# Optimization experiments

Measured on AMD Instinct MI355X. Metric: run time of the kernel, lower is better.

The kernel has to match this reference:

```python
import jax, jax.numpy as jnp
import numpy as np

N_NODES = 50000
N_EDGES = 800000
N_GRAPHS = 128


def gcn_conv(x, row, col, W, b, num_nodes):
    # GCNConv: x' = D^-1/2 (A + I) D^-1/2 (x W) + b, with self-loops added.
    h = x @ W  # [N, out]
    # append self-loops
    sl = jnp.arange(num_nodes, dtype=row.dtype)
    r = jnp.concatenate([row, sl])
    c = jnp.concatenate([col, sl])
    deg = jax.ops.segment_sum(jnp.ones_like(r, dtype=h.dtype), r, num_segments=num_nodes)
    dinv = jnp.where(deg > 0, jax.lax.rsqrt(deg), 0.0)
    norm = dinv[r] * dinv[c]  # [E+N]
    msg = h[c] * norm[:, None]  # gather + scale
    out = jax.ops.segment_sum(msg, r, num_segments=num_nodes)
    return out + b


def setup_inputs() -> dict:
    key = jax.random.key(0)
    k = jax.random.split(key, 6)
    x = jax.random.normal(k[0], (N_NODES, 256), dtype=jnp.float32)
    edge_index = jax.random.randint(k[1], (2, N_EDGES), 0, N_NODES, dtype=jnp.int32)
    batch = jnp.sort(jax.random.randint(k[2], (N_NODES,), 0, N_GRAPHS, dtype=jnp.int32))
    W1 = jax.random.normal(k[3], (256, 128), dtype=jnp.float32) * (1.0 / np.sqrt(256))
    b1 = jnp.zeros((128,), dtype=jnp.float32)
    W2 = jax.random.normal(k[4], (128, 32), dtype=jnp.float32) * (1.0 / np.sqrt(128))
    b2 = jnp.zeros((32,), dtype=jnp.float32)
    return {"x": x, "edge_index": edge_index, "batch": batch,
            "W1": W1, "b1": b1, "W2": W2, "b2": b2}


def reference(x, edge_index, batch, W1, b1, W2, b2):
    row, col = edge_index[0], edge_index[1]
    h = gcn_conv(x, row, col, W1, b1, N_NODES)
    h = jax.nn.relu(h)
    # dropout is identity in eval mode (training=False)
    h = gcn_conv(h, row, col, W2, b2, N_NODES)
    # global_mean_pool over batch ids
    sums = jax.ops.segment_sum(h, batch, num_segments=N_GRAPHS)
    cnts = jax.ops.segment_sum(jnp.ones((N_NODES,), dtype=h.dtype), batch, num_segments=N_GRAPHS)
    pooled = sums / jnp.clip(cnts, 1.0)[:, None]  # [G, num_classes]
    return jax.nn.log_softmax(pooled, axis=1)
```

## Files before the change

kernel.cpp:

```cpp
#include <hip/hip_runtime.h>
#include <math.h>

#define N_NODES 50000
#define N_EDGES 800000
#define N_GRAPHS 128
#define DIM0 256
#define DIM1 128
#define DIM2 32

#define NBUCK 196
#define NEB 98

using f32x4 = __attribute__((ext_vector_type(4))) float;
using s16x8 = __attribute__((ext_vector_type(8))) short;

__device__ inline unsigned bf16pack(float a, float b) {
    unsigned ua = __float_as_uint(a), ub = __float_as_uint(b);
    ua = (ua + 0x7fffu + ((ua >> 16) & 1u)) >> 16;
    ub = (ub + 0x7fffu + ((ub >> 16) & 1u)) >> 16;
    return ua | (ub << 16);
}
__device__ inline float2 bf16x2(unsigned p) {
    return make_float2(__uint_as_float(p << 16), __uint_as_float(p & 0xffff0000u));
}

__global__ __launch_bounds__(256) void k_preph(const float* __restrict__ W1, uint* __restrict__ W1b,
                                               const int* __restrict__ batch, int* gstart,
                                               const int* __restrict__ row, int* __restrict__ hist) {
    __shared__ int h[NBUCK];
    int b = blockIdx.x, t = threadIdx.x;
    if (b < NEB) {
        if (t < NBUCK) h[t] = 0;
        __syncthreads();
#pragma unroll
        for (int i = 0; i < 8; ++i) {
            int idx = b * 2048 + i * 256 + t;
            if (idx < N_EDGES / 4) {
                int4 r4 = ((const int4*)row)[idx];
                atomicAdd(&h[r4.x >> 8], 1);
                atomicAdd(&h[r4.y >> 8], 1);
                atomicAdd(&h[r4.z >> 8], 1);
                atomicAdd(&h[r4.w >> 8], 1);
            }
        }
        __syncthreads();
        if (t < NBUCK) hist[b * NBUCK + t] = h[t];
    } else {
        int g = (b - NEB) * 256 + t;
        {
            int s = g >> 9, tt = (g >> 6) & 7, q = (g >> 4) & 3, n = g & 15;
            int k0 = s * 32 + q * 8;
            int col = tt * 16 + n;
            uint4 o;
            o.x = bf16pack(W1[(size_t)(k0 + 0) * DIM1 + col], W1[(size_t)(k0 + 1) * DIM1 + col]);
            o.y = bf16pack(W1[(size_t)(k0 + 2) * DIM1 + col], W1[(size_t)(k0 + 3) * DIM1 + col]);
            o.z = bf16pack(W1[(size_t)(k0 + 4) * DIM1 + col], W1[(size_t)(k0 + 5) * DIM1 + col]);
            o.w = bf16pack(W1[(size_t)(k0 + 6) * DIM1 + col], W1[(size_t)(k0 + 7) * DIM1 + col]);
            ((uint4*)W1b)[g] = o;
        }
        if (g <= N_GRAPHS) {
            int lo = 0, hi = N_NODES;
            while (lo < hi) { int mid = (lo + hi) >> 1; if (batch[mid] < g) lo = mid + 1; else hi = mid; }
            gstart[g] = lo;
        }
    }
}

__global__ __launch_bounds__(256) void k_place(const int* __restrict__ row, const int* __restrict__ col,
                                               const int* __restrict__ hist, uint* __restrict__ bb,
                                               int* __restrict__ bbase, int* __restrict__ btot) {
    __shared__ int cur[NBUCK];
    __shared__ int tot[NBUCK];
    __shared__ int sc[256];
    int blk = blockIdx.x, t = threadIdx.x;
    int pre = 0, to = 0;
    for (int b2 = 0; b2 < NEB; ++b2) {
        int v = (t < NBUCK) ? hist[b2 * NBUCK + t] : 0;
        to += v;
        if (b2 < blk) pre += v;
    }
    if (t < NBUCK) tot[t] = to;
    sc[t] = (t < NBUCK) ? to : 0;
    __syncthreads();
    for (int off = 1; off < 256; off <<= 1) {
        int x = (t >= off) ? sc[t - off] : 0;
        __syncthreads();
        sc[t] += x;
        __syncthreads();
    }
    if (t < NBUCK) {
        int base = sc[t] - tot[t];
        cur[t] = base + pre;
        if (blk == 0) { bbase[t] = base; btot[t] = tot[t]; }
    }
    __syncthreads();
#pragma unroll
    for (int i = 0; i < 8; ++i) {
        int idx = blk * 2048 + i * 256 + t;
        if (idx < N_EDGES / 4) {
            int4 r4 = ((const int4*)row)[idx];
            int4 c4 = ((const int4*)col)[idx];
            int rs[4] = {r4.x, r4.y, r4.z, r4.w};
            int cs[4] = {c4.x, c4.y, c4.z, c4.w};
#pragma unroll
            for (int j = 0; j < 4; ++j) {
                int pos = atomicAdd(&cur[rs[j] >> 8], 1);
                bb[pos] = ((uint)(rs[j] & 255) << 16) | (uint)cs[j];
            }
        }
    }
}

__global__ __launch_bounds__(256) void k_build(const int* __restrict__ bbase, const int* __restrict__ btot,
                                               const uint* __restrict__ bb,
                                               int* __restrict__ offs, int* __restrict__ cnt,
                                               ushort* __restrict__ csr) {
    __shared__ int c256[256];
    __shared__ int cur256[256];
    __shared__ int wsum[4];
    int b = blockIdx.x, t = threadIdx.x;
    int start = bbase[b];
    int n = btot[b];
    c256[t] = 0;
    __syncthreads();
    for (int i = t; i < n; i += 256) atomicAdd(&c256[bb[start + i] >> 16], 1);
    __syncthreads();
    int w = t >> 6, l = t & 63;
    int v = c256[t];
    int incl = v;
#pragma unroll
    for (int off = 1; off < 64; off <<= 1) {
        int x = __shfl_up(incl, off, 64);
        if (l >= off) incl += x;
    }
    if (l == 63) wsum[w] = incl;
    __syncthreads();
    int woff = 0;
    for (int i = 0; i < w; ++i) woff += wsum[i];
    int excl = incl - v + woff;
    cur256[t] = excl;
    int r = b * 256 + t;
    if (r < N_NODES) { offs[r] = start + excl; cnt[r] = v; }
    __syncthreads();
    for (int i = t; i < n; i += 256) {
        uint e = bb[start + i];
        int pos = atomicAdd(&cur256[e >> 16], 1);
        csr[start + pos] = (ushort)(e & 0xFFFFu);
    }
}

#define G1_BM 128
#define AS_LD 20
__global__ __launch_bounds__(256) void k_gemm1(const float* __restrict__ X, const uint* __restrict__ W1b,
                                               const int* __restrict__ cnt, unsigned* __restrict__ h1u) {
    __shared__ uint w1s[16384];
    __shared__ uint As[G1_BM * AS_LD];
    int t = threadIdx.x;
    int w = t >> 6, lane = t & 63, q = lane >> 4, m16 = lane & 15;
    int rowBase = blockIdx.x * G1_BM;

    {
        const uint4* src = (const uint4*)W1b;
        uint4* dst = (uint4*)w1s;
#pragma unroll
        for (int i = 0; i < 16; ++i) dst[i * 256 + t] = src[i * 256 + t];
    }

    f32x4 acc[2][8];
#pragma unroll
    for (int i = 0; i < 2; ++i)
#pragma unroll
        for (int j = 0; j < 8; ++j) acc[i][j] = (f32x4){0.f, 0.f, 0.f, 0.f};

    int ar = t >> 1, ah = t & 1;
    for (int s = 0; s < 8; ++s) {
        float4 f0 = {0,0,0,0}, f1 = {0,0,0,0}, f2 = {0,0,0,0}, f3 = {0,0,0,0};
        int grow = rowBase + ar;
        if (grow < N_NODES) {
            const float* src = X + (size_t)grow * DIM0 + s * 32 + ah * 16;
            f0 = *(const float4*)(src + 0);
            f1 = *(const float4*)(src + 4);
            f2 = *(const float4*)(src + 8);
            f3 = *(const float4*)(src + 12);
        }
        uint4 p0, p1;
        p0.x = bf16pack(f0.x, f0.y); p0.y = bf16pack(f0.z, f0.w);
        p0.z = bf16pack(f1.x, f1.y); p0.w = bf16pack(f1.z, f1.w);
        p1.x = bf16pack(f2.x, f2.y); p1.y = bf16pack(f2.z, f2.w);
        p1.z = bf16pack(f3.x, f3.y); p1.w = bf16pack(f3.z, f3.w);
        __syncthreads();
        *(uint4*)&As[ar * AS_LD + ah * 8 + 0] = p0;
        *(uint4*)&As[ar * AS_LD + ah * 8 + 4] = p1;
        __syncthreads();

        s16x8 af[2];
#pragma unroll
        for (int rt = 0; rt < 2; ++rt) {
            int arow = w * 32 + rt * 16 + m16;
            af[rt] = *(s16x8*)&As[arow * AS_LD + q * 4];
        }
#pragma unroll
        for (int tt = 0; tt < 8; ++tt) {
            s16x8 bf = *(s16x8*)&w1s[((s * 8 + tt) * 64 + lane) * 4];
            acc[0][tt] = __builtin_amdgcn_mfma_f32_16x16x32_bf16(af[0], bf, acc[0][tt], 0, 0, 0);
            acc[1][tt] = __builtin_amdgcn_mfma_f32_16x16x32_bf16(af[1], bf, acc[1][tt], 0, 0, 0);
        }
    }

#pragma unroll
    for (int rt = 0; rt < 2; ++rt) {
#pragma unroll
        for (int reg = 0; reg < 4; ++reg) {
            int row = rowBase + w * 32 + rt * 16 + q * 4 + reg;
            if (row < N_NODES) {
                float dv = rsqrtf((float)(cnt[row] + 1));
                unsigned* hr = h1u + (size_t)row * 64;
#pragma unroll
                for (int u = 0; u < 4; ++u)
                    hr[u * 16 + m16] = bf16pack(acc[rt][2 * u][reg] * dv, acc[rt][2 * u + 1][reg] * dv);
            }
        }
    }
}

__global__ __launch_bounds__(256) void k_agg1(const unsigned* __restrict__ h1u, const int* __restrict__ cnt,
                                              const int* __restrict__ offs, const ushort* __restrict__ csr,
                                              const float* __restrict__ b1, unsigned* __restrict__ a1u) {
    int node = blockIdx.x * 4 + (threadIdx.x >> 6);
    int lane = threadIdx.x & 63;
    float2 acc = bf16x2(h1u[(size_t)node * 64 + lane]);
    int n = cnt[node];
    const ushort* cp = csr + offs[node];
    {
        int ec = 0;
        if (lane < n) ec = cp[lane];
        int j = 0;
        for (; j + 8 <= n; j += 8) {
            int c0 = __shfl(ec, j),     c1 = __shfl(ec, j + 1), c2 = __shfl(ec, j + 2), c3 = __shfl(ec, j + 3);
            int c4 = __shfl(ec, j + 4), c5 = __shfl(ec, j + 5), c6 = __shfl(ec, j + 6), c7 = __shfl(ec, j + 7);
            unsigned p0 = h1u[(size_t)c0 * 64 + lane];
            unsigned p1 = h1u[(size_t)c1 * 64 + lane];
            unsigned p2 = h1u[(size_t)c2 * 64 + lane];
            unsigned p3 = h1u[(size_t)c3 * 64 + lane];
            unsigned p4 = h1u[(size_t)c4 * 64 + lane];
            unsigned p5 = h1u[(size_t)c5 * 64 + lane];
            unsigned p6 = h1u[(size_t)c6 * 64 + lane];
            unsigned p7 = h1u[(size_t)c7 * 64 + lane];
            float2 v0 = bf16x2(p0), v1 = bf16x2(p1), v2 = bf16x2(p2), v3 = bf16x2(p3);
            float2 v4 = bf16x2(p4), v5 = bf16x2(p5), v6 = bf16x2(p6), v7 = bf16x2(p7);
            acc.x += (v0.x + v1.x) + (v2.x + v3.x) + (v4.x + v5.x) + (v6.x + v7.x);
            acc.y += (v0.y + v1.y) + (v2.y + v3.y) + (v4.y + v5.y) + (v6.y + v7.y);
        }
        for (; j + 4 <= n; j += 4) {
            int c0 = __shfl(ec, j), c1 = __shfl(ec, j + 1), c2 = __shfl(ec, j + 2), c3 = __shfl(ec, j + 3);
            unsigned p0 = h1u[(size_t)c0 * 64 + lane];
            unsigned p1 = h1u[(size_t)c1 * 64 + lane];
            unsigned p2 = h1u[(size_t)c2 * 64 + lane];
            unsigned p3 = h1u[(size_t)c3 * 64 + lane];
            float2 v0 = bf16x2(p0), v1 = bf16x2(p1), v2 = bf16x2(p2), v3 = bf16x2(p3);
            acc.x += (v0.x + v1.x) + (v2.x + v3.x);
            acc.y += (v0.y + v1.y) + (v2.y + v3.y);
        }
        for (; j < n; ++j) {
            int c = __shfl(ec, j);
            float2 v = bf16x2(h1u[(size_t)c * 64 + lane]);
            acc.x += v.x; acc.y += v.y;
        }
    }
    float di = rsqrtf((float)(n + 1));
    int f0 = (lane >> 4) * 32 + (lane & 15);
    acc.x = fmaxf(acc.x * di + b1[f0], 0.f);
    acc.y = fmaxf(acc.y * di + b1[f0 + 16], 0.f);
    a1u[(size_t)node * 64 + lane] = bf16pack(acc.x, acc.y);
}

#define AS2_LD 132
__global__ __launch_bounds__(256) void k_gemm2(const unsigned* __restrict__ a1u, const float* __restrict__ W2,
                                               const int* __restrict__ cnt, unsigned* __restrict__ h2u) {
    __shared__ float As2[16 * AS2_LD];
    __shared__ float W2s[DIM1 * DIM2];
    int t = threadIdx.x;
    int rb = blockIdx.x * 16;
    {
        int r = t >> 4, cb = (t & 15) * 8;
        uint4 pv = *(const uint4*)(a1u + (size_t)(rb + r) * 64 + (t & 15) * 4);
        float2 u0 = bf16x2(pv.x), u1 = bf16x2(pv.y), u2 = bf16x2(pv.z), u3 = bf16x2(pv.w);
        float* dst = &As2[r * AS2_LD + cb];
        dst[0] = u0.x; dst[1] = u0.y; dst[2] = u1.x; dst[3] = u1.y;
        dst[4] = u2.x; dst[5] = u2.y; dst[6] = u3.x; dst[7] = u3.y;
    }
    for (int i = t; i < 1024; i += 256) {
        int k = i >> 3, c4 = (i & 7) * 4;
        int pos = 2 * ((k >> 5) * 16 + (k & 15)) + ((k >> 4) & 1);
        *(float4*)&W2s[pos * DIM2 + c4] = *(const float4*)(W2 + (size_t)k * DIM2 + c4);
    }
    __syncthreads();
    int r = t >> 4, c2 = (t & 15) * 2;
    float a0 = 0.f, a1v = 0.f;
#pragma unroll 8
    for (int k = 0; k < DIM1; ++k) {
        float a_ = As2[r * AS2_LD + k];
        a0  += a_ * W2s[k * DIM2 + c2];
        a1v += a_ * W2s[k * DIM2 + c2 + 1];
    }
    float dv = rsqrtf((float)(cnt[rb + r] + 1));
    h2u[(size_t)(rb + r) * 16 + (t & 15)] = bf16pack(a0 * dv, a1v * dv);
}

__global__ __launch_bounds__(256) void k_agg2(const unsigned* __restrict__ h2u, const int* __restrict__ cnt,
                                              const int* __restrict__ offs, const ushort* __restrict__ csr,
                                              const float* __restrict__ b2, float* __restrict__ a2) {
    int t = threadIdx.x;
    int node = blockIdx.x * 16 + (t >> 4);
    int l = t & 15;
    float2 acc = bf16x2(h2u[(size_t)node * 16 + l]);
    int n = cnt[node];
    const ushort* cp = csr + offs[node];
    for (int base = 0; base < n; base += 16) {
        int m = min(16, n - base);
        int ec = 0;
        if (l < m) ec = cp[base + l];
        int j = 0;
        for (; j + 4 <= m; j += 4) {
            int c0 = __shfl(ec, j, 16), c1 = __shfl(ec, j + 1, 16);
            int c2 = __shfl(ec, j + 2, 16), c3 = __shfl(ec, j + 3, 16);
            unsigned p0 = h2u[(size_t)c0 * 16 + l];
            unsigned p1 = h2u[(size_t)c1 * 16 + l];
            unsigned p2 = h2u[(size_t)c2 * 16 + l];
            unsigned p3 = h2u[(size_t)c3 * 16 + l];
            float2 v0 = bf16x2(p0), v1 = bf16x2(p1), v2 = bf16x2(p2), v3 = bf16x2(p3);
            acc.x += v0.x + v1.x + v2.x + v3.x;
            acc.y += v0.y + v1.y + v2.y + v3.y;
        }
        for (; j < m; ++j) {
            int c = __shfl(ec, j, 16);
            float2 v = bf16x2(h2u[(size_t)c * 16 + l]);
            acc.x += v.x; acc.y += v.y;
        }
    }
    float di = rsqrtf((float)(n + 1));
    acc.x = acc.x * di + b2[2 * l];
    acc.y = acc.y * di + b2[2 * l + 1];
    ((float2*)a2)[(size_t)node * 16 + l] = acc;
}

__global__ __launch_bounds__(256) void k_pool(const float* __restrict__ a2, const int* __restrict__ gstart,
                                              float* __restrict__ out) {
    __shared__ float sred[8][DIM2];
    int g = blockIdx.x;
    int t = threadIdx.x;
    int s = gstart[g], e = gstart[g + 1];
    int d = t & 31, r = t >> 5;
    float acc = 0.f;
    for (int i = s + r; i < e; i += 8) acc += a2[(size_t)i * DIM2 + d];
    sred[r][d] = acc;
    __syncthreads();
    if (t < DIM2) {
        float sum = 0.f;
#pragma unroll
        for (int j = 0; j < 8; ++j) sum += sred[j][t];
        float cntf = fmaxf((float)(e - s), 1.0f);
        float val = sum / cntf;
        float v = val;
#pragma unroll
        for (int m = 16; m >= 1; m >>= 1) v = fmaxf(v, __shfl_xor(v, m, 32));
        float ex = expf(val - v);
#pragma unroll
        for (int m = 16; m >= 1; m >>= 1) ex += __shfl_xor(ex, m, 32);
        out[g * DIM2 + t] = val - v - logf(ex);
    }
}

extern "C" void kernel_launch(void* const* d_in, const int* in_sizes, int n_in,
                              void* d_out, int out_size, void* d_ws, size_t ws_size,
                              hipStream_t stream) {
    const float* x     = (const float*)d_in[0];
    const int*   eidx  = (const int*)d_in[1];
    const int*   batch = (const int*)d_in[2];
    const float* W1    = (const float*)d_in[3];
    const float* b1    = (const float*)d_in[4];
    const float* W2    = (const float*)d_in[5];
    const float* b2    = (const float*)d_in[6];
    const int* row = eidx;
    const int* col = eidx + N_EDGES;
    float* out = (float*)d_out;

    char* p = (char*)d_ws;
    int*    cnt    = (int*)p;    p += (size_t)N_NODES * 4;
    int*    offs   = (int*)p;    p += (size_t)N_NODES * 4 + 16;
    int*    gstart = (int*)p;    p += 768;
    uint*   W1b    = (uint*)p;   p += 4096 * 16;
    int*    hist   = (int*)p;    p += (size_t)NEB * NBUCK * 4 + 32;
    int*    bbase  = (int*)p;    p += 1024;
    int*    btot   = (int*)p;    p += 1024;
    uint*   bb     = (uint*)p;   p += (size_t)N_EDGES * 4;
    ushort* csr    = (ushort*)p; p += (size_t)N_EDGES * 2;
    unsigned* h1u  = (unsigned*)p; p += (size_t)N_NODES * 64 * 4;
    unsigned* a1u  = (unsigned*)p; p += (size_t)N_NODES * 64 * 4;
    unsigned* h2u  = (unsigned*)p; p += (size_t)N_NODES * 16 * 4;
    float*  a2     = (float*)p;  p += (size_t)N_NODES * DIM2 * 4;

    k_preph<<<NEB + 16, 256, 0, stream>>>(W1, W1b, batch, gstart, row, hist);
    k_place<<<NEB, 256, 0, stream>>>(row, col, hist, bb, bbase, btot);
    k_build<<<NBUCK, 256, 0, stream>>>(bbase, btot, bb, offs, cnt, csr);

    k_gemm1<<<(N_NODES + G1_BM - 1) / G1_BM, 256, 0, stream>>>(x, W1b, cnt, h1u);
    k_agg1<<<N_NODES / 4, 256, 0, stream>>>(h1u, cnt, offs, csr, b1, a1u);
    k_gemm2<<<N_NODES / 16, 256, 0, stream>>>(a1u, W2, cnt, h2u);
    k_agg2<<<N_NODES / 16, 256, 0, stream>>>(h2u, cnt, offs, csr, b2, a2);
    k_pool<<<N_GRAPHS, 256, 0, stream>>>(a2, gstart, out);
}
```

Measured before the change: 225.8 us.

## Fuse layer-1 aggregation with layer-2 GEMM using bf16 MFMA

Merges k_agg1 and k_gemm2 into one kernel. Each block aggregates 16 nodes into an LDS tile, then one wave multiplies the tile by a pre-packed bf16 W2 using MFMA 16x16x32 instructions. This removes the a1u global round trip and one launch, and moves the second GEMM from scalar FP32 to bf16 MFMA. Output features come out permuted, so the agg2 bias indexing and the pool output write are remapped to match. Costs: 4x fewer, larger blocks for the aggregation and only one wave active during the GEMM phase.

Result: faster. 204.6 us (-9.4%).

```diff
diff --git a/kernel.cpp b/kernel.cpp
--- a/kernel.cpp
+++ b/kernel.cpp
@@ -24,7 +24,12 @@
     return make_float2(__uint_as_float(p << 16), __uint_as_float(p & 0xffff0000u));
 }
 
+__device__ inline int featOf(int p) {
+    return 32 * (p >> 5) + ((p >> 1) & 15) + 16 * (p & 1);
+}
+
 __global__ __launch_bounds__(256) void k_preph(const float* __restrict__ W1, uint* __restrict__ W1b,
+                                               const float* __restrict__ W2, uint* __restrict__ W2b,
                                                const int* __restrict__ batch, int* gstart,
                                                const int* __restrict__ row, int* __restrict__ hist) {
     __shared__ int h[NBUCK];
@@ -58,6 +63,17 @@
             o.w = bf16pack(W1[(size_t)(k0 + 6) * DIM1 + col], W1[(size_t)(k0 + 7) * DIM1 + col]);
             ((uint4*)W1b)[g] = o;
         }
+        if (g < 512) {
+            int s = g >> 7, tt = (g >> 6) & 1, l = g & 63;
+            int n = tt * 16 + (l & 15);
+            int kb = s * 32 + (l >> 4) * 8;
+            uint4 o;
+            o.x = bf16pack(W2[(size_t)featOf(kb + 0) * DIM2 + n], W2[(size_t)featOf(kb + 1) * DIM2 + n]);
+            o.y = bf16pack(W2[(size_t)featOf(kb + 2) * DIM2 + n], W2[(size_t)featOf(kb + 3) * DIM2 + n]);
+            o.z = bf16pack(W2[(size_t)featOf(kb + 4) * DIM2 + n], W2[(size_t)featOf(kb + 5) * DIM2 + n]);
+            o.w = bf16pack(W2[(size_t)featOf(kb + 6) * DIM2 + n], W2[(size_t)featOf(kb + 7) * DIM2 + n]);
+            ((uint4*)W2b)[g] = o;
+        }
         if (g <= N_GRAPHS) {
             int lo = 0, hi = N_NODES;
             while (lo < hi) { int mid = (lo + hi) >> 1; if (batch[mid] < g) lo = mid + 1; else hi = mid; }
@@ -223,15 +239,24 @@
     }
 }
 
-__global__ __launch_bounds__(256) void k_agg1(const unsigned* __restrict__ h1u, const int* __restrict__ cnt,
-                                              const int* __restrict__ offs, const ushort* __restrict__ csr,
-                                              const float* __restrict__ b1, unsigned* __restrict__ a1u) {
-    int node = blockIdx.x * 4 + (threadIdx.x >> 6);
-    int lane = threadIdx.x & 63;
-    float2 acc = bf16x2(h1u[(size_t)node * 64 + lane]);
-    int n = cnt[node];
-    const ushort* cp = csr + offs[node];
-    {
+#define A1_LD 68
+__global__ __launch_bounds__(256) void k_agg1g2(const unsigned* __restrict__ h1u, const int* __restrict__ cnt,
+                                                const int* __restrict__ offs, const ushort* __restrict__ csr,
+                                                const float* __restrict__ b1, const uint* __restrict__ W2b,
+                                                unsigned* __restrict__ h2u) {
+    __shared__ uint a1tile[16 * A1_LD];
+    __shared__ float sdi[16];
+    int t = threadIdx.x;
+    int wv = t >> 6, lane = t & 63;
+    int nb16 = blockIdx.x * 16;
+
+#pragma unroll
+    for (int i = 0; i < 4; ++i) {
+        int m = wv * 4 + i;
+        int node = nb16 + m;
+        float2 acc = bf16x2(h1u[(size_t)node * 64 + lane]);
+        int n = cnt[node];
+        const ushort* cp = csr + offs[node];
         int ec = 0;
         if (lane < n) ec = cp[lane];
         int j = 0;
@@ -266,45 +291,34 @@
             float2 v = bf16x2(h1u[(size_t)c * 64 + lane]);
             acc.x += v.x; acc.y += v.y;
         }
-    }
-    float di = rsqrtf((float)(n + 1));
-    int f0 = (lane >> 4) * 32 + (lane & 15);
-    acc.x = fmaxf(acc.x * di + b1[f0], 0.f);
-    acc.y = fmaxf(acc.y * di + b1[f0 + 16], 0.f);
-    a1u[(size_t)node * 64 + lane] = bf16pack(acc.x, acc.y);
-}
-
-#define AS2_LD 132
-__global__ __launch_bounds__(256) void k_gemm2(const unsigned* __restrict__ a1u, const float* __restrict__ W2,
-                                               const int* __restrict__ cnt, unsigned* __restrict__ h2u) {
-    __shared__ float As2[16 * AS2_LD];
-    __shared__ float W2s[DIM1 * DIM2];
-    int t = threadIdx.x;
-    int rb = blockIdx.x * 16;
-    {
-        int r = t >> 4, cb = (t & 15) * 8;
-        uint4 pv = *(const uint4*)(a1u + (size_t)(rb + r) * 64 + (t & 15) * 4);
-        float2 u0 = bf16x2(pv.x), u1 = bf16x2(pv.y), u2 = bf16x2(pv.z), u3 = bf16x2(pv.w);
-        float* dst = &As2[r * AS2_LD + cb];
-        dst[0] = u0.x; dst[1] = u0.y; dst[2] = u1.x; dst[3] = u1.y;
-        dst[4] = u2.x; dst[5] = u2.y; dst[6] = u3.x; dst[7] = u3.y;
-    }
-    for (int i = t; i < 1024; i += 256) {
-        int k = i >> 3, c4 = (i & 7) * 4;
-        int pos = 2 * ((k >> 5) * 16 + (k & 15)) + ((k >> 4) & 1);
-        *(float4*)&W2s[pos * DIM2 + c4] = *(const float4*)(W2 + (size_t)k * DIM2 + c4);
-    }
-    __syncthreads();
-    int r = t >> 4, c2 = (t & 15) * 2;
-    float a0 = 0.f, a1v = 0.f;
-#pragma unroll 8
-    for (int k = 0; k < DIM1; ++k) {
-        float a_ = As2[r * AS2_LD + k];
-        a0  += a_ * W2s[k * DIM2 + c2];
-        a1v += a_ * W2s[k * DIM2 + c2 + 1];
-    }
-    float dv = rsqrtf((float)(cnt[rb + r] + 1));
-    h2u[(size_t)(rb + r) * 16 + (t & 15)] = bf16pack(a0 * dv, a1v * dv);
+        float di = rsqrtf((float)(n + 1));
+        if (lane == 0) sdi[m] = di;
+        int f0 = (lane >> 4) * 32 + (lane & 15);
+        acc.x = fmaxf(acc.x * di + b1[f0], 0.f);
+        acc.y = fmaxf(acc.y * di + b1[f0 + 16], 0.f);
+        a1tile[m * A1_LD + lane] = bf16pack(acc.x, acc.y);
+    }
+    __syncthreads();
+
+    if (wv == 0) {
+        int q = lane >> 4, m16 = lane & 15;
+        f32x4 accA = (f32x4){0.f, 0.f, 0.f, 0.f};
+        f32x4 accB = (f32x4){0.f, 0.f, 0.f, 0.f};
+#pragma unroll
+        for (int s = 0; s < 4; ++s) {
+            s16x8 af = *(s16x8*)&a1tile[m16 * A1_LD + s * 16 + q * 4];
+            s16x8 bf0 = *(const s16x8*)(W2b + (size_t)((s * 2 + 0) * 64 + lane) * 4);
+            s16x8 bf1 = *(const s16x8*)(W2b + (size_t)((s * 2 + 1) * 64 + lane) * 4);
+            accA = __builtin_amdgcn_mfma_f32_16x16x32_bf16(af, bf0, accA, 0, 0, 0);
+            accB = __builtin_amdgcn_mfma_f32_16x16x32_bf16(af, bf1, accB, 0, 0, 0);
+        }
+#pragma unroll
+        for (int r = 0; r < 4; ++r) {
+            int node = nb16 + q * 4 + r;
+            float dv = sdi[q * 4 + r];
+            h2u[(size_t)node * 16 + m16] = bf16pack(accA[r] * dv, accB[r] * dv);
+        }
+    }
 }
 
 __global__ __launch_bounds__(256) void k_agg2(const unsigned* __restrict__ h2u, const int* __restrict__ cnt,
@@ -339,8 +353,8 @@
         }
     }
     float di = rsqrtf((float)(n + 1));
-    acc.x = acc.x * di + b2[2 * l];
-    acc.y = acc.y * di + b2[2 * l + 1];
+    acc.x = acc.x * di + b2[l];
+    acc.y = acc.y * di + b2[l + 16];
     ((float2*)a2)[(size_t)node * 16 + l] = acc;
 }
 
@@ -367,7 +381,8 @@
         float ex = expf(val - v);
 #pragma unroll
         for (int m = 16; m >= 1; m >>= 1) ex += __shfl_xor(ex, m, 32);
-        out[g * DIM2 + t] = val - v - logf(ex);
+        int feat = (t >> 1) + 16 * (t & 1);
+        out[g * DIM2 + feat] = val - v - logf(ex);
     }
 }
 
@@ -390,23 +405,22 @@
     int*    offs   = (int*)p;    p += (size_t)N_NODES * 4 + 16;
     int*    gstart = (int*)p;    p += 768;
     uint*   W1b    = (uint*)p;   p += 4096 * 16;
+    uint*   W2b    = (uint*)p;   p += 512 * 16;
     int*    hist   = (int*)p;    p += (size_t)NEB * NBUCK * 4 + 32;
     int*    bbase  = (int*)p;    p += 1024;
     int*    btot   = (int*)p;    p += 1024;
     uint*   bb     = (uint*)p;   p += (size_t)N_EDGES * 4;
     ushort* csr    = (ushort*)p; p += (size_t)N_EDGES * 2;
     unsigned* h1u  = (unsigned*)p; p += (size_t)N_NODES * 64 * 4;
-    unsigned* a1u  = (unsigned*)p; p += (size_t)N_NODES * 64 * 4;
     unsigned* h2u  = (unsigned*)p; p += (size_t)N_NODES * 16 * 4;
     float*  a2     = (float*)p;  p += (size_t)N_NODES * DIM2 * 4;
 
-    k_preph<<<NEB + 16, 256, 0, stream>>>(W1, W1b, batch, gstart, row, hist);
+    k_preph<<<NEB + 16, 256, 0, stream>>>(W1, W1b, W2, W2b, batch, gstart, row, hist);
     k_place<<<NEB, 256, 0, stream>>>(row, col, hist, bb, bbase, btot);
     k_build<<<NBUCK, 256, 0, stream>>>(bbase, btot, bb, offs, cnt, csr);
 
     k_gemm1<<<(N_NODES + G1_BM - 1) / G1_BM, 256, 0, stream>>>(x, W1b, cnt, h1u);
-    k_agg1<<<N_NODES / 4, 256, 0, stream>>>(h1u, cnt, offs, csr, b1, a1u);
-    k_gemm2<<<N_NODES / 16, 256, 0, stream>>>(a1u, W2, cnt, h2u);
+    k_agg1g2<<<N_NODES / 16, 256, 0, stream>>>(h1u, cnt, offs, csr, b1, W2b, h2u);
     k_agg2<<<N_NODES / 16, 256, 0, stream>>>(h2u, cnt, offs, csr, b2, a2);
     k_pool<<<N_GRAPHS, 256, 0, stream>>>(a2, gstart, out);
 }
```
